# Performance work log

Hardware: AMD Instinct MI355X
Metric: run time of the kernel (lower is better)

Reference implementation:

```python
import jax, jax.numpy as jnp
import numpy as np

N_QUBITS = 16
N_BLOCKS = 8
N_ADDR_QUBITS = 4  # (8).bit_length() -> min(n_qubits, bit_length)
N_HEADS = 16


def setup_inputs() -> dict:
    key = jax.random.key(0)
    ks = jax.random.split(key, 9)
    B, S, D, M, J, Q = 4, 2048, 1024, 2048, N_BLOCKS, N_QUBITS
    s = lambda d: 1.0 / np.sqrt(d)
    return {
        "query": jax.random.normal(ks[0], (B, S, D), jnp.float32),
        "W_addr": jax.random.normal(ks[1], (D, Q), jnp.float32) * s(D),
        "b_addr": jnp.zeros((Q,), jnp.float32),
        "memory": jax.random.normal(ks[2], (J, M), jnp.float32),
        "W_out": jax.random.normal(ks[3], (M, D), jnp.float32) * s(M),
        "b_out": jnp.zeros((D,), jnp.float32),
        "Wq": jax.random.normal(ks[4], (D, D), jnp.float32) * s(D),
        "bq": jnp.zeros((D,), jnp.float32),
        "Wk": jax.random.normal(ks[5], (D, D), jnp.float32) * s(D),
        "bk": jnp.zeros((D,), jnp.float32),
        "Wv": jax.random.normal(ks[6], (D, D), jnp.float32) * s(D),
        "bv": jnp.zeros((D,), jnp.float32),
        "Wo": jax.random.normal(ks[7], (D, D), jnp.float32) * s(D),
        "bo": jnp.zeros((D,), jnp.float32),
    }


def _address_weights(query, W_addr, b_addr):
    # Deterministic expectation of the per-token quantum register loop:
    # RX(theta) applied iff theta > 0 -> P(measure 1) = sin^2(theta/2), else 0.
    theta = query @ W_addr + b_addr                      # [B,S,Q]
    p1 = jnp.where(theta > 0, jnp.sin(theta * 0.5) ** 2, 0.0)
    p = p1[..., :N_ADDR_QUBITS]                          # only bit_length(J) qubits used
    bits = ((jnp.arange(N_BLOCKS)[:, None] >> jnp.arange(N_ADDR_QUBITS)[None, :]) & 1
            ).astype(query.dtype)                        # [J, Qa]
    # score[b,s,j] = sum_q [ bits*p + (1-bits)*(1-p) ]
    scores = jnp.einsum("bsq,jq->bsj", p, bits) + jnp.einsum("bsq,jq->bsj", 1.0 - p, 1.0 - bits)
    return jax.nn.softmax(scores, axis=-1)               # [B,S,J]


def reference(query, W_addr, b_addr, memory, W_out, b_out,
              Wq, bq, Wk, bk, Wv, bv, Wo, bo):
    addr = _address_weights(query, W_addr, b_addr)       # [B,S,J]
    mem_read = jnp.einsum("bsj,jm->bsm", addr, memory)   # [B,S,M]
    out = mem_read @ W_out + b_out                       # [B,S,D]

    # quantum_attention(q=k=v=out): multi-head self-attention
    B, S, D = out.shape
    hd = D // N_HEADS
    q = (out @ Wq + bq).reshape(B, S, N_HEADS, hd)
    k = (out @ Wk + bk).reshape(B, S, N_HEADS, hd)
    v = (out @ Wv + bv).reshape(B, S, N_HEADS, hd)
    att = jax.nn.softmax(jnp.einsum("bihd,bjhd->bhij", q, k) / np.sqrt(hd), axis=-1)
    ctx = jnp.einsum("bhij,bjhd->bihd", att, v).reshape(B, S, D)
    return ctx @ Wo + bo
```

## Files before the change

### kernel.cpp

```cpp
#include <hip/hip_runtime.h>

#define B_ 4
#define S_ 2048
#define D_ 1024
#define M_ 2048
#define J_ 8
#define H_ 16
#define HD_ 64
#define BH_ 64

typedef __attribute__((ext_vector_type(8))) short short8;
typedef __attribute__((ext_vector_type(4))) float f32x4;
typedef __attribute__((ext_vector_type(16))) float f32x16;

static __device__ __forceinline__ unsigned short f2bf(float x) {
  unsigned u = __float_as_uint(x);
  u = u + 0x7fffu + ((u >> 16) & 1u);
  return (unsigned short)(u >> 16);
}

static __device__ __forceinline__ unsigned cvtpk(float lo, float hi) {
  unsigned r;
  asm("v_cvt_pk_bf16_f32 %0, %1, %2" : "=v"(r) : "v"(lo), "v"(hi));
  return r;
}

static __device__ __forceinline__ void gload16(const void* g, void* l) {
  __builtin_amdgcn_global_load_lds(
      (const __attribute__((address_space(1))) unsigned*)g,
      (__attribute__((address_space(3))) unsigned*)l, 16, 0, 0);
}

__global__ __launch_bounds__(256) void k_mw_part(const float* __restrict__ memory,
                                                 const float* __restrict__ W_out,
                                                 float* __restrict__ part) {
  int nc = blockIdx.x >> 4, ks = blockIdx.x & 15;
  int t = threadIdx.x;
  int n = nc * 64 + (t & 63);
  int sub = t >> 6;
  int k0 = ks * 128 + sub * 32;
  float acc[J_];
#pragma unroll
  for (int j = 0; j < J_; ++j) acc[j] = 0.f;
  for (int k = k0; k < k0 + 32; ++k) {
    float wv = W_out[(size_t)k * D_ + n];
#pragma unroll
    for (int j = 0; j < J_; ++j) acc[j] += memory[j * M_ + k] * wv;
  }
  __shared__ float p4[4][J_][64];
#pragma unroll
  for (int j = 0; j < J_; ++j) p4[sub][j][t & 63] = acc[j];
  __syncthreads();
  if (t < 64) {
#pragma unroll
    for (int j = 0; j < J_; ++j)
      part[((size_t)ks * J_ + j) * D_ + nc * 64 + t] =
          p4[0][j][t] + p4[1][j][t] + p4[2][j][t] + p4[3][j][t];
  }
}

__global__ __launch_bounds__(256) void k_mw_red(const float* __restrict__ part,
                                                const float* __restrict__ b_out,
                                                const float* __restrict__ W_addr,
                                                float* __restrict__ G,
                                                float* __restrict__ WaT) {
  if (blockIdx.x >= 36) {
    int q = blockIdx.x - 36;
    int c = threadIdx.x * 4;
#pragma unroll
    for (int e = 0; e < 4; ++e) WaT[q * D_ + c + e] = W_addr[(size_t)(c + e) * 16 + q];
    return;
  }
  int id = blockIdx.x * 256 + threadIdx.x;
  int j = id >> 10, n = id & 1023;
  if (j < 8) {
    float s = 0.f;
#pragma unroll
    for (int ks = 0; ks < 16; ++ks) s += part[((size_t)ks * J_ + j) * D_ + n];
    G[j * D_ + n] = s;
  } else {
    G[8 * D_ + n] = b_out[n];
  }
}

__global__ __launch_bounds__(256) void k_mwq_part(const float* __restrict__ G,
                                                  const float* __restrict__ Wq,
                                                  const float* __restrict__ Wk,
                                                  const float* __restrict__ Wv,
                                                  float* __restrict__ partq) {
  int wi = blockIdx.x >> 6;
  int r = blockIdx.x & 63;
  int nc = r & 15, ks = r >> 4;
  const float* W = wi == 0 ? Wq : (wi == 1 ? Wk : Wv);
  int t = threadIdx.x;
  int n = nc * 64 + (t & 63);
  int sub = t >> 6;
  int k0 = ks * 256 + sub * 64;
  float acc[9];
#pragma unroll
  for (int j = 0; j < 9; ++j) acc[j] = 0.f;
  for (int k = k0; k < k0 + 64; ++k) {
    float wv = W[(size_t)k * D_ + n];
#pragma unroll
    for (int j = 0; j < 9; ++j) acc[j] += G[j * D_ + k] * wv;
  }
  __shared__ float p4[4][9][64];
#pragma unroll
  for (int j = 0; j < 9; ++j) p4[sub][j][t & 63] = acc[j];
  __syncthreads();
  if (t < 64) {
#pragma unroll
    for (int j = 0; j < 9; ++j)
      partq[(((size_t)wi * 4 + ks) * 9 + j) * D_ + nc * 64 + t] =
          p4[0][j][t] + p4[1][j][t] + p4[2][j][t] + p4[3][j][t];
  }
}

__global__ __launch_bounds__(256) void k_mwq_red(const float* __restrict__ partq,
                                                 const float* __restrict__ bq,
                                                 const float* __restrict__ bk,
                                                 const float* __restrict__ bv,
                                                 float* __restrict__ Hq,
                                                 float* __restrict__ Hk,
                                                 float* __restrict__ Hv) {
  int id = blockIdx.x * 256 + threadIdx.x;
  int wi = id / 9216;
  int rem = id - wi * 9216;
  int j = rem >> 10, n = rem & 1023;
  float s = 0.f;
#pragma unroll
  for (int ks = 0; ks < 4; ++ks)
    s += partq[(((size_t)wi * 4 + ks) * 9 + j) * D_ + n];
  if (j == 8) s += wi == 0 ? bq[n] : (wi == 1 ? bk[n] : bv[n]);
  float* Hh = wi == 0 ? Hq : (wi == 1 ? Hk : Hv);
  Hh[j * D_ + n] = s;
}

__global__ __launch_bounds__(256) void k_wot(const float* __restrict__ Wo,
                                             unsigned short* __restrict__ WoT) {
  int kt = blockIdx.x, nt = blockIdx.y;
  int t = threadIdx.x;
  __shared__ float tl[64][65];
  int r = t >> 6, c = t & 63;
#pragma unroll
  for (int i = 0; i < 16; ++i) {
    int row = i * 4 + r;
    tl[row][c] = Wo[(size_t)(kt * 64 + row) * D_ + nt * 64 + c];
  }
  __syncthreads();
#pragma unroll
  for (int i = 0; i < 16; ++i) {
    int nrow = i * 4 + r;
    WoT[(size_t)(nt * 64 + nrow) * D_ + kt * 64 + c] = f2bf(tl[c][nrow]);
  }
}

__global__ __launch_bounds__(256) void k_qkv(
    const float* __restrict__ query, const float* __restrict__ WaT,
    const float* __restrict__ b_addr, const float* __restrict__ Hq,
    const float* __restrict__ Hk, const float* __restrict__ Hv,
    unsigned short* __restrict__ Qg, unsigned short* __restrict__ Kg,
    unsigned short* __restrict__ Vg) {
  int w = threadIdx.x >> 6, l = threadIdx.x & 63;
  int tk = blockIdx.x * 4 + w;
  int b = tk >> 11, s = tk & (S_ - 1);
  const float* qrow = query + (size_t)tk * D_;
  float th0 = 0.f, th1 = 0.f, th2 = 0.f, th3 = 0.f;
#pragma unroll
  for (int e = 0; e < 4; ++e) {
    float4 qv = *(const float4*)(qrow + e * 256 + l * 4);
    float4 w0 = *(const float4*)(WaT + 0 * D_ + e * 256 + l * 4);
    float4 w1 = *(const float4*)(WaT + 1 * D_ + e * 256 + l * 4);
    float4 w2 = *(const float4*)(WaT + 2 * D_ + e * 256 + l * 4);
    float4 w3 = *(const float4*)(WaT + 3 * D_ + e * 256 + l * 4);
    th0 += qv.x * w0.x + qv.y * w0.y + qv.z * w0.z + qv.w * w0.w;
    th1 += qv.x * w1.x + qv.y * w1.y + qv.z * w1.z + qv.w * w1.w;
    th2 += qv.x * w2.x + qv.y * w2.y + qv.z * w2.z + qv.w * w2.w;
    th3 += qv.x * w3.x + qv.y * w3.y + qv.z * w3.z + qv.w * w3.w;
  }
#pragma unroll
  for (int off = 32; off; off >>= 1) {
    th0 += __shfl_xor(th0, off);
    th1 += __shfl_xor(th1, off);
    th2 += __shfl_xor(th2, off);
    th3 += __shfl_xor(th3, off);
  }
  float thv[4] = {th0 + b_addr[0], th1 + b_addr[1], th2 + b_addr[2],
                  th3 + b_addr[3]};
  float p[4];
#pragma unroll
  for (int q = 0; q < 4; ++q) {
    float sh = __sinf(thv[q] * 0.5f);
    p[q] = thv[q] > 0.f ? sh * sh : 0.f;
  }
  float sc[8];
  float mx = -1e30f;
#pragma unroll
  for (int j = 0; j < 8; ++j) {
    float v = 0.f;
#pragma unroll
    for (int q = 0; q < 4; ++q) v += ((j >> q) & 1) ? p[q] : 1.f - p[q];
    sc[j] = v;
    mx = fmaxf(mx, v);
  }
  float sum = 0.f;
#pragma unroll
  for (int j = 0; j < 8; ++j) {
    sc[j] = __expf(sc[j] - mx);
    sum += sc[j];
  }
  float inv = 1.f / sum;
  float a[8];
#pragma unroll
  for (int j = 0; j < 8; ++j) a[j] = sc[j] * inv;

  const float* Hs[3] = {Hq, Hk, Hv};
  unsigned short* os[3] = {Qg, Kg, Vg};
#pragma unroll
  for (int k = 0; k < 4; ++k) {
    int n0 = k * 256 + l * 4;
    int hh = n0 >> 6, d = n0 & 63;
    size_t obase = ((size_t)(b * H_ + hh) * S_ + s) * HD_ + d;
#pragma unroll
    for (int wi = 0; wi < 3; ++wi) {
      const float* Hh = Hs[wi];
      float4 accv = *(const float4*)(Hh + 8 * D_ + n0);
#pragma unroll
      for (int j = 0; j < 8; ++j) {
        float4 hv = *(const float4*)(Hh + j * D_ + n0);
        accv.x += a[j] * hv.x;
        accv.y += a[j] * hv.y;
        accv.z += a[j] * hv.z;
        accv.w += a[j] * hv.w;
      }
      uint2 pk;
      pk.x = (unsigned)f2bf(accv.x) | ((unsigned)f2bf(accv.y) << 16);
      pk.y = (unsigned)f2bf(accv.z) | ((unsigned)f2bf(accv.w) << 16);
      *(uint2*)(os[wi] + obase) = pk;
    }
  }
}

__global__ __launch_bounds__(256) void k_vt(const unsigned short* __restrict__ Vg,
                                            unsigned short* __restrict__ Vtg) {
  int st = blockIdx.x & 31, bh = blockIdx.x >> 5;
  int t = threadIdx.x;
  __shared__ unsigned short tl[64][65];
  int rr = t >> 3, c8 = t & 7;
#pragma unroll
  for (int p = 0; p < 2; ++p) {
    int s = p * 32 + rr;
    uint4 v = *(const uint4*)(Vg + ((size_t)bh * S_ + st * 64 + s) * HD_ + c8 * 8);
    const unsigned short* pv = (const unsigned short*)&v;
#pragma unroll
    for (int j = 0; j < 8; ++j) tl[s][c8 * 8 + j] = pv[j];
  }
  __syncthreads();
#pragma unroll
  for (int p = 0; p < 2; ++p) {
    int d = p * 32 + rr;
    unsigned short o[8];
#pragma unroll
    for (int j = 0; j < 8; ++j) o[j] = tl[c8 * 8 + j][d];
    *(uint4*)(Vtg + ((size_t)bh * HD_ + d) * S_ + st * 64 + c8 * 8) = *(const uint4*)o;
  }
}

__global__ __launch_bounds__(512, 4) void k_attn(
    const unsigned short* __restrict__ Qg, const unsigned short* __restrict__ Kg,
    const unsigned short* __restrict__ Vtg, unsigned short* __restrict__ ctxg) {
  int id = blockIdx.x;
  int xcd = id & 7;
  int qt = (id >> 3) & 15;
  int bh = xcd * 8 + (id >> 7);
  int t = threadIdx.x;
  int w = t >> 6, l = t & 63;
  int q31 = l & 31, h = l >> 5;
  int g = w >> 2;

  __shared__ __align__(16) unsigned short lds[32768];

  int q0 = qt * 128;
  const unsigned short* qp = Qg + ((size_t)bh * S_ + q0 + (w & 3) * 32 + q31) * HD_;
  short8 qf0 = *(const short8*)(qp + 0 + h * 8);
  short8 qf1 = *(const short8*)(qp + 16 + h * 8);
  short8 qf2 = *(const short8*)(qp + 32 + h * 8);
  short8 qf3 = *(const short8*)(qp + 48 + h * 8);

  f32x16 accO0 = {}, accO1 = {};
  float lsum = 0.f;

  const unsigned short* kgb = Kg + (size_t)bh * S_ * HD_;
  const unsigned short* vtb = Vtg + (size_t)bh * HD_ * S_;
  int wg = w & 3;
  int rowK = l >> 3, gsl = l & 7;
  int srcg = gsl ^ rowK;

  {
    unsigned short* sKd = lds + g * 8192;
    unsigned short* sVd = sKd + 4096;
#pragma unroll
    for (int cc = 0; cc < 2; ++cc) {
      int c = wg * 2 + cc;
      int rr = c * 8 + rowK;
      gload16(kgb + ((size_t)(g * 1024 + rr)) * HD_ + srcg * 8, sKd + c * 512);
      gload16(vtb + (size_t)rr * S_ + g * 1024 + srcg * 8, sVd + c * 512);
    }
  }
  __syncthreads();

  const float K1 = 0.125f * 1.44269504f;
  const float M2 = 28.8539008f;

  for (int it = 0; it < 16; ++it) {
    if (it < 15) {
      int kvn = g * 1024 + (it + 1) * 64;
      unsigned short* sKd = lds + ((it + 1) & 1) * 16384 + g * 8192;
      unsigned short* sVd = sKd + 4096;
#pragma unroll
      for (int cc = 0; cc < 2; ++cc) {
        int c = wg * 2 + cc;
        int rr = c * 8 + rowK;
        gload16(kgb + (size_t)(kvn + rr) * HD_ + srcg * 8, sKd + c * 512);
        gload16(vtb + (size_t)rr * S_ + kvn + srcg * 8, sVd + c * 512);
      }
    }
    unsigned short* sK = lds + (it & 1) * 16384 + g * 8192;
    unsigned short* sVt = sK + 4096;

    f32x16 accS0 = {}, accS1 = {};
    __builtin_amdgcn_s_setprio(1);
#pragma unroll
    for (int ds = 0; ds < 4; ++ds) {
      short8 qq = ds == 0 ? qf0 : ds == 1 ? qf1 : ds == 2 ? qf2 : qf3;
      {
        int row = q31;
        int gk = (ds * 2 + h) ^ (row & 7);
        short8 kf = *(const short8*)(sK + row * 64 + gk * 8);
        accS0 = __builtin_amdgcn_mfma_f32_32x32x16_bf16(kf, qq, accS0, 0, 0, 0);
      }
      {
        int row = 32 + q31;
        int gk = (ds * 2 + h) ^ (row & 7);
        short8 kf = *(const short8*)(sK + row * 64 + gk * 8);
        accS1 = __builtin_amdgcn_mfma_f32_32x32x16_bf16(kf, qq, accS1, 0, 0, 0);
      }
    }
    __builtin_amdgcn_s_setprio(0);

    float ts = 0.f;
#pragma unroll
    for (int r = 0; r < 16; ++r) {
      float p0 = __builtin_exp2f(accS0[r] * K1 - M2);
      float p1 = __builtin_exp2f(accS1[r] * K1 - M2);
      accS0[r] = p0;
      accS1[r] = p1;
      ts += p0 + p1;
    }
    lsum += ts;

    short8 pb[4];
#pragma unroll
    for (int ks = 0; ks < 4; ++ks) {
      const int r0 = 8 * (ks & 1);
      float v0, v1, v2, v3, v4, v5, v6, v7;
      if (ks < 2) {
        v0 = accS0[r0 + 0]; v1 = accS0[r0 + 1]; v2 = accS0[r0 + 2]; v3 = accS0[r0 + 3];
        v4 = accS0[r0 + 4]; v5 = accS0[r0 + 5]; v6 = accS0[r0 + 6]; v7 = accS0[r0 + 7];
      } else {
        v0 = accS1[r0 + 0]; v1 = accS1[r0 + 1]; v2 = accS1[r0 + 2]; v3 = accS1[r0 + 3];
        v4 = accS1[r0 + 4]; v5 = accS1[r0 + 5]; v6 = accS1[r0 + 6]; v7 = accS1[r0 + 7];
      }
      unsigned X0 = cvtpk(v0, v1), X1 = cvtpk(v2, v3);
      unsigned Y0 = cvtpk(v4, v5), Y1 = cvtpk(v6, v7);
      union { unsigned u[4]; short8 s8; } uu;
#if __has_builtin(__builtin_amdgcn_permlane32_swap)
      typedef __attribute__((ext_vector_type(2))) unsigned uint2v;
      uint2v r02 = __builtin_amdgcn_permlane32_swap(X0, Y0, false, false);
      uint2v r13 = __builtin_amdgcn_permlane32_swap(X1, Y1, false, false);
      uu.u[0] = r02[0]; uu.u[1] = r13[0]; uu.u[2] = r02[1]; uu.u[3] = r13[1];
#else
      unsigned tX0 = __shfl_xor(X0, 32), tX1 = __shfl_xor(X1, 32);
      unsigned tY0 = __shfl_xor(Y0, 32), tY1 = __shfl_xor(Y1, 32);
      uu.u[0] = h ? tY0 : X0;
      uu.u[1] = h ? tY1 : X1;
      uu.u[2] = h ? Y0 : tX0;
      uu.u[3] = h ? Y1 : tX1;
#endif
      pb[ks] = uu.s8;
    }

    __builtin_amdgcn_s_setprio(1);
    {
      int row = q31;
      int rs = row & 7;
#pragma unroll
      for (int ks = 0; ks < 4; ++ks) {
        int gv = (ks * 2 + h) ^ rs;
        short8 vf = *(const short8*)(sVt + row * 64 + gv * 8);
        accO0 = __builtin_amdgcn_mfma_f32_32x32x16_bf16(vf, pb[ks], accO0, 0, 0, 0);
      }
    }
    {
      int row = 32 + q31;
      int rs = row & 7;
#pragma unroll
      for (int ks = 0; ks < 4; ++ks) {
        int gv = (ks * 2 + h) ^ rs;
        short8 vf = *(const short8*)(sVt + row * 64 + gv * 8);
        accO1 = __builtin_amdgcn_mfma_f32_32x32x16_bf16(vf, pb[ks], accO1, 0, 0, 0);
      }
    }
    __builtin_amdgcn_s_setprio(0);

    __syncthreads();
  }

  float lt = lsum + __shfl_xor(lsum, 32);

  if (g == 1) {
    unsigned* xO = (unsigned*)lds;
    int base = ((w & 3) * 64 + l) * 17;
#pragma unroll
    for (int j = 0; j < 8; ++j) xO[base + j] = cvtpk(accO0[2 * j], accO0[2 * j + 1]);
#pragma unroll
    for (int j = 0; j < 8; ++j) xO[base + 8 + j] = cvtpk(accO1[2 * j], accO1[2 * j + 1]);
    float* xml = (float*)(lds + 8704);
    if (h == 0) xml[(w & 3) * 32 + q31] = lt;
  }
  __syncthreads();
  float inv = 0.f;
  if (g == 0) {
    unsigned* xO = (unsigned*)lds;
    float* xml = (float*)(lds + 8704);
    int base = (w * 64 + l) * 17;
    inv = 1.f / (lt + xml[w * 32 + q31]);
#pragma unroll
    for (int j = 0; j < 8; ++j) {
      unsigned wd = xO[base + j];
      accO0[2 * j] += __uint_as_float(wd << 16);
      accO0[2 * j + 1] += __uint_as_float(wd & 0xffff0000u);
    }
#pragma unroll
    for (int j = 0; j < 8; ++j) {
      unsigned wd = xO[base + 8 + j];
      accO1[2 * j] += __uint_as_float(wd << 16);
      accO1[2 * j + 1] += __uint_as_float(wd & 0xffff0000u);
    }
  }
  __syncthreads();
  if (g == 0) {
    int row = w * 32 + q31;
    int swz = (q31 & 7) << 3;
#pragma unroll
    for (int r = 0; r < 16; ++r) {
      int dl = (r & 3) + 8 * (r >> 2) + 4 * h;
      lds[row * 64 + (dl ^ swz)] = f2bf(accO0[r] * inv);
      lds[row * 64 + ((32 + dl) ^ swz)] = f2bf(accO1[r] * inv);
    }
  }
  __syncthreads();
  int b = bh >> 4, head = bh & 15;
#pragma unroll
  for (int j = 0; j < 2; ++j) {
    int slot = t + j * 512;
    int row = slot >> 3, gg = slot & 7;
    uint4 vv = *(const uint4*)(lds + row * 64 + ((gg ^ (row & 7)) * 8));
    *(uint4*)(ctxg + ((size_t)(b * S_ + q0 + row)) * D_ + head * HD_ + gg * 8) = vv;
  }
}

__global__ __launch_bounds__(256) void k_out(const unsigned short* __restrict__ Ag,
                                             const unsigned short* __restrict__ Btg,
                                             const float* __restrict__ bo,
                                             float* __restrict__ out) {
  int mt = blockIdx.x;
  int nt = blockIdx.y;
  int t = threadIdx.x;
  int w = t >> 6, l = t & 63;
  int l15 = l & 15, l4 = l >> 4;
  int wr = w >> 1, wc = w & 1;
  __shared__ __align__(16) unsigned short sA[128 * 64];
  __shared__ __align__(16) unsigned short sB[128 * 64];
  f32x4 acc[4][4];
#pragma unroll
  for (int mm = 0; mm < 4; ++mm)
#pragma unroll
    for (int nn = 0; nn < 4; ++nn) acc[mm][nn] = (f32x4){0.f, 0.f, 0.f, 0.f};
  int srow = t >> 3, sc8 = t & 7;
  for (int kt = 0; kt < 16; ++kt) {
    int k0 = kt * 64;
    __syncthreads();
#pragma unroll
    for (int p = 0; p < 4; ++p) {
      int row = p * 32 + srow;
      int di = row * 64 + ((sc8 * 8) ^ ((row & 7) << 3));
      *(uint4*)(sA + di) =
          *(const uint4*)(Ag + (size_t)(mt * 128 + row) * D_ + k0 + sc8 * 8);
      *(uint4*)(sB + di) =
          *(const uint4*)(Btg + (size_t)(nt * 128 + row) * D_ + k0 + sc8 * 8);
    }
    __syncthreads();
    short8 a[4][2];
#pragma unroll
    for (int mm = 0; mm < 4; ++mm) {
      int row = wr * 64 + mm * 16 + l15;
      int sw = (row & 7) << 3;
      a[mm][0] = *(const short8*)(sA + row * 64 + ((l4 * 8) ^ sw));
      a[mm][1] = *(const short8*)(sA + row * 64 + ((32 + l4 * 8) ^ sw));
    }
#pragma unroll
    for (int nn = 0; nn < 4; ++nn) {
      int row = wc * 64 + nn * 16 + l15;
      int sw = (row & 7) << 3;
      short8 b0 = *(const short8*)(sB + row * 64 + ((l4 * 8) ^ sw));
      short8 b1 = *(const short8*)(sB + row * 64 + ((32 + l4 * 8) ^ sw));
#pragma unroll
      for (int mm = 0; mm < 4; ++mm) {
        acc[mm][nn] = __builtin_amdgcn_mfma_f32_16x16x32_bf16(a[mm][0], b0, acc[mm][nn], 0, 0, 0);
        acc[mm][nn] = __builtin_amdgcn_mfma_f32_16x16x32_bf16(a[mm][1], b1, acc[mm][nn], 0, 0, 0);
      }
    }
  }
#pragma unroll
  for (int mm = 0; mm < 4; ++mm) {
#pragma unroll
    for (int r = 0; r < 4; ++r) {
      int mrow = mt * 128 + wr * 64 + mm * 16 + l4 * 4 + r;
      float* orow = out + (size_t)mrow * D_ + nt * 128 + wc * 64;
#pragma unroll
      for (int nn = 0; nn < 4; ++nn) {
        int n = nn * 16 + l15;
        orow[n] = acc[mm][nn][r] + bo[nt * 128 + wc * 64 + n];
      }
    }
  }
}

extern "C" void kernel_launch(void* const* d_in, const int* in_sizes, int n_in,
                              void* d_out, int out_size, void* d_ws, size_t ws_size,
                              hipStream_t stream) {
  const float* query = (const float*)d_in[0];
  const float* W_addr = (const float*)d_in[1];
  const float* b_addr = (const float*)d_in[2];
  const float* memory = (const float*)d_in[3];
  const float* W_out = (const float*)d_in[4];
  const float* b_out = (const float*)d_in[5];
  const float* Wq = (const float*)d_in[6];
  const float* bq = (const float*)d_in[7];
  const float* Wk = (const float*)d_in[8];
  const float* bk = (const float*)d_in[9];
  const float* Wv = (const float*)d_in[10];
  const float* bv = (const float*)d_in[11];
  const float* Wo = (const float*)d_in[12];
  const float* bo = (const float*)d_in[13];
  float* out = (float*)d_out;

  char* ws = (char*)d_ws;
  size_t off = 0;
  auto alloc = [&](size_t bytes) {
    char* p = ws + off;
    off = (off + bytes + 255) & ~(size_t)255;
    return p;
  };
  float* G = (float*)alloc(9 * D_ * sizeof(float));
  float* HqA = (float*)alloc(9 * D_ * sizeof(float));
  float* HkA = (float*)alloc(9 * D_ * sizeof(float));
  float* HvA = (float*)alloc(9 * D_ * sizeof(float));
  float* WaT = (float*)alloc(4 * D_ * sizeof(float));
  float* partmw = (float*)alloc(16 * J_ * D_ * sizeof(float));
  float* partq = (float*)alloc(3 * 4 * 9 * D_ * sizeof(float));
  unsigned short* WoT = (unsigned short*)alloc((size_t)D_ * D_ * 2);
  unsigned short* Vg = (unsigned short*)alloc((size_t)BH_ * S_ * HD_ * 2);
  unsigned short* Vtg = (unsigned short*)alloc((size_t)BH_ * S_ * HD_ * 2);
  unsigned short* Qg = (unsigned short*)d_out;
  unsigned short* Kg = Qg + (size_t)BH_ * S_ * HD_;
  unsigned short* ctx = Vg;

  k_mw_part<<<256, 256, 0, stream>>>(memory, W_out, partmw);
  k_mw_red<<<40, 256, 0, stream>>>(partmw, b_out, W_addr, G, WaT);
  k_mwq_part<<<192, 256, 0, stream>>>(G, Wq, Wk, Wv, partq);
  k_mwq_red<<<108, 256, 0, stream>>>(partq, bq, bk, bv, HqA, HkA, HvA);
  k_wot<<<dim3(16, 16), 256, 0, stream>>>(Wo, WoT);
  k_qkv<<<B_ * S_ / 4, 256, 0, stream>>>(query, WaT, b_addr, HqA, HkA, HvA,
                                         Qg, Kg, Vg);
  k_vt<<<BH_ * 32, 256, 0, stream>>>(Vg, Vtg);
  k_attn<<<1024, 512, 0, stream>>>(Qg, Kg, Vtg, ctx);
  k_out<<<dim3(64, 8), 256, 0, stream>>>(ctx, WoT, bo, out);
}
```

Before: 232.7 us.

## Merge Wo transpose into mw_part, MFMA row sums, async LDS loads in k_out

```diff
diff --git a/kernel.cpp b/kernel.cpp
--- a/kernel.cpp
+++ b/kernel.cpp
@@ -33,7 +33,28 @@
 
 __global__ __launch_bounds__(256) void k_mw_part(const float* __restrict__ memory,
                                                  const float* __restrict__ W_out,
-                                                 float* __restrict__ part) {
+                                                 const float* __restrict__ Wo,
+                                                 float* __restrict__ part,
+                                                 unsigned short* __restrict__ WoT) {
+  if (blockIdx.x >= 256) {
+    int idx = blockIdx.x - 256;
+    int kt = idx & 15, nt = idx >> 4;
+    int t = threadIdx.x;
+    __shared__ float tl[64][65];
+    int r = t >> 6, c = t & 63;
+#pragma unroll
+    for (int i = 0; i < 16; ++i) {
+      int row = i * 4 + r;
+      tl[row][c] = Wo[(size_t)(kt * 64 + row) * D_ + nt * 64 + c];
+    }
+    __syncthreads();
+#pragma unroll
+    for (int i = 0; i < 16; ++i) {
+      int nrow = i * 4 + r;
+      WoT[(size_t)(nt * 64 + nrow) * D_ + kt * 64 + c] = f2bf(tl[c][nrow]);
+    }
+    return;
+  }
   int nc = blockIdx.x >> 4, ks = blockIdx.x & 15;
   int t = threadIdx.x;
   int n = nc * 64 + (t & 63);
@@ -136,25 +157,6 @@
   Hh[j * D_ + n] = s;
 }
 
-__global__ __launch_bounds__(256) void k_wot(const float* __restrict__ Wo,
-                                             unsigned short* __restrict__ WoT) {
-  int kt = blockIdx.x, nt = blockIdx.y;
-  int t = threadIdx.x;
-  __shared__ float tl[64][65];
-  int r = t >> 6, c = t & 63;
-#pragma unroll
-  for (int i = 0; i < 16; ++i) {
-    int row = i * 4 + r;
-    tl[row][c] = Wo[(size_t)(kt * 64 + row) * D_ + nt * 64 + c];
-  }
-  __syncthreads();
-#pragma unroll
-  for (int i = 0; i < 16; ++i) {
-    int nrow = i * 4 + r;
-    WoT[(size_t)(nt * 64 + nrow) * D_ + kt * 64 + c] = f2bf(tl[c][nrow]);
-  }
-}
-
 __global__ __launch_bounds__(256) void k_qkv(
     const float* __restrict__ query, const float* __restrict__ WaT,
     const float* __restrict__ b_addr, const float* __restrict__ Hq,
@@ -287,8 +289,11 @@
   short8 qf2 = *(const short8*)(qp + 32 + h * 8);
   short8 qf3 = *(const short8*)(qp + 48 + h * 8);
 
-  f32x16 accO0 = {}, accO1 = {};
-  float lsum = 0.f;
+  short8 onesv;
+#pragma unroll
+  for (int e = 0; e < 8; ++e) onesv[e] = (short)0x3F80;
+
+  f32x16 accO0 = {}, accO1 = {}, accL = {};
 
   const unsigned short* kgb = Kg + (size_t)bh * S_ * HD_;
   const unsigned short* vtb = Vtg + (size_t)bh * HD_ * S_;
@@ -348,16 +353,11 @@
     }
     __builtin_amdgcn_s_setprio(0);
 
-    float ts = 0.f;
 #pragma unroll
     for (int r = 0; r < 16; ++r) {
-      float p0 = __builtin_exp2f(accS0[r] * K1 - M2);
-      float p1 = __builtin_exp2f(accS1[r] * K1 - M2);
-      accS0[r] = p0;
-      accS1[r] = p1;
-      ts += p0 + p1;
-    }
-    lsum += ts;
+      accS0[r] = __builtin_exp2f(accS0[r] * K1 - M2);
+      accS1[r] = __builtin_exp2f(accS1[r] * K1 - M2);
+    }
 
     short8 pb[4];
 #pragma unroll
@@ -399,6 +399,7 @@
         int gv = (ks * 2 + h) ^ rs;
         short8 vf = *(const short8*)(sVt + row * 64 + gv * 8);
         accO0 = __builtin_amdgcn_mfma_f32_32x32x16_bf16(vf, pb[ks], accO0, 0, 0, 0);
+        accL = __builtin_amdgcn_mfma_f32_32x32x16_bf16(onesv, pb[ks], accL, 0, 0, 0);
       }
     }
     {
@@ -416,7 +417,7 @@
     __syncthreads();
   }
 
-  float lt = lsum + __shfl_xor(lsum, 32);
+  float lt = accL[0];
 
   if (g == 1) {
     unsigned* xO = (unsigned*)lds;
@@ -487,18 +488,18 @@
   for (int mm = 0; mm < 4; ++mm)
 #pragma unroll
     for (int nn = 0; nn < 4; ++nn) acc[mm][nn] = (f32x4){0.f, 0.f, 0.f, 0.f};
-  int srow = t >> 3, sc8 = t & 7;
+  int srow = t >> 3, gsl = t & 7;
+  int srcg = gsl ^ (srow & 7);
   for (int kt = 0; kt < 16; ++kt) {
     int k0 = kt * 64;
     __syncthreads();
 #pragma unroll
     for (int p = 0; p < 4; ++p) {
       int row = p * 32 + srow;
-      int di = row * 64 + ((sc8 * 8) ^ ((row & 7) << 3));
-      *(uint4*)(sA + di) =
-          *(const uint4*)(Ag + (size_t)(mt * 128 + row) * D_ + k0 + sc8 * 8);
-      *(uint4*)(sB + di) =
-          *(const uint4*)(Btg + (size_t)(nt * 128 + row) * D_ + k0 + sc8 * 8);
+      gload16(Ag + (size_t)(mt * 128 + row) * D_ + k0 + srcg * 8,
+              sA + (p * 256 + t) * 8);
+      gload16(Btg + (size_t)(nt * 128 + row) * D_ + k0 + srcg * 8,
+              sB + (p * 256 + t) * 8);
     }
     __syncthreads();
     short8 a[4][2];
@@ -577,11 +578,10 @@
   unsigned short* Kg = Qg + (size_t)BH_ * S_ * HD_;
   unsigned short* ctx = Vg;
 
-  k_mw_part<<<256, 256, 0, stream>>>(memory, W_out, partmw);
+  k_mw_part<<<512, 256, 0, stream>>>(memory, W_out, Wo, partmw, WoT);
   k_mw_red<<<40, 256, 0, stream>>>(partmw, b_out, W_addr, G, WaT);
   k_mwq_part<<<192, 256, 0, stream>>>(G, Wq, Wk, Wv, partq);
   k_mwq_red<<<108, 256, 0, stream>>>(partq, bq, bk, bv, HqA, HkA, HvA);
-  k_wot<<<dim3(16, 16), 256, 0, stream>>>(Wo, WoT);
   k_qkv<<<B_ * S_ / 4, 256, 0, stream>>>(query, WaT, b_addr, HqA, HkA, HvA,
                                          Qg, Kg, Vg);
   k_vt<<<BH_ * 32, 256, 0, stream>>>(Vg, Vtg);
```

After: 235.3 us. Within noise of the previous version (+1.1%).
